# Optimization experiments

Measured on AMD Instinct MI355X. Metric: run time of the kernel, lower is better.

## Reference

```python
import jax, jax.numpy as jnp
import numpy as np

B, L, DIM = 4, 8192, 512
HEADS, WIN = 8, 256
HID = int(DIM * 4.0)
HEAD_DIM = DIM // HEADS
EPS = 1e-5


def _layernorm(x, g, b):
    m = jnp.mean(x, axis=-1, keepdims=True)
    v = jnp.mean(jnp.square(x - m), axis=-1, keepdims=True)
    return (x - m) * jax.lax.rsqrt(v + EPS) * g + b


def setup_inputs() -> dict:
    key = jax.random.key(0)
    ks = jax.random.split(key, 8)
    s = 0.02
    return {
        "x": jax.random.normal(ks[0], (B, L, DIM), jnp.float32),
        "norm1_g": jnp.ones((DIM,), jnp.float32),
        "norm1_b": jnp.zeros((DIM,), jnp.float32),
        "qkv_w": jax.random.normal(ks[1], (DIM, 3 * DIM), jnp.float32) * s,
        "qkv_b": jnp.zeros((3 * DIM,), jnp.float32),
        "rpb_table": jax.random.normal(ks[2], (2 * WIN - 1, HEADS), jnp.float32) * s,
        "proj_w": jax.random.normal(ks[3], (DIM, DIM), jnp.float32) * s,
        "proj_b": jnp.zeros((DIM,), jnp.float32),
        "norm2_g": jnp.ones((DIM,), jnp.float32),
        "norm2_b": jnp.zeros((DIM,), jnp.float32),
        "fc1_w": jax.random.normal(ks[4], (DIM, HID), jnp.float32) * s,
        "fc1_b": jnp.zeros((HID,), jnp.float32),
        "fc2_w": jax.random.normal(ks[5], (HID, DIM), jnp.float32) * s,
        "fc2_b": jnp.zeros((DIM,), jnp.float32),
    }


def reference(x, norm1_g, norm1_b, qkv_w, qkv_b, rpb_table, proj_w, proj_b,
              norm2_g, norm2_b, fc1_w, fc1_b, fc2_w, fc2_b):
    scale = HEAD_DIM ** -0.5
    nW = L // WIN
    BW = B * nW

    shortcut = x
    h = _layernorm(x, norm1_g, norm1_b)
    xw = h.reshape(BW, WIN, DIM)

    qkv = (xw @ qkv_w + qkv_b).reshape(BW, WIN, 3, HEADS, HEAD_DIM)
    q = jnp.moveaxis(qkv[:, :, 0], 1, 2) * scale  # (BW, H, W, d)
    k = jnp.moveaxis(qkv[:, :, 1], 1, 2)
    v = jnp.moveaxis(qkv[:, :, 2], 1, 2)

    attn = jnp.einsum('bhqd,bhkd->bhqk', q, k)
    # relative position bias gather: (W, W, H) -> (H, W, W)
    coords = jnp.arange(WIN)
    ridx = coords[:, None] - coords[None, :] + WIN - 1
    bias = rpb_table[ridx]  # (W, W, H)
    attn = attn + jnp.transpose(bias, (2, 0, 1))[None]
    attn = jax.nn.softmax(attn, axis=-1)

    out = jnp.einsum('bhqk,bhkd->bhqd', attn, v)  # (BW, H, W, d)
    out = jnp.moveaxis(out, 1, 2).reshape(BW, WIN, DIM)
    out = out @ proj_w + proj_b

    x = shortcut + out.reshape(B, L, DIM)
    # NOTE: norm2 output feeds BOTH the residual branch and the MLP (as in source)
    x = _layernorm(x, norm2_g, norm2_b)
    m = jax.nn.gelu(x @ fc1_w + fc1_b, approximate=False) @ fc2_w + fc2_b
    return x + m
```

## Files before the change

### kernel.cpp

```cpp
#include <hip/hip_runtime.h>
#include <hip/hip_bf16.h>
#include <math.h>
#include <stdint.h>


typedef __attribute__((ext_vector_type(8))) __bf16 bf16x8;
typedef __attribute__((ext_vector_type(4))) __bf16 bf16x4;
typedef __attribute__((ext_vector_type(4))) float  f32x4;

#define NTOK  32768
#define DIMC  512
#define HEADS 8
#define WIN   256
#define HD    64
#define HIDC  2048
#define LDP   40

__device__ __forceinline__ void gld16(const __bf16* g, __bf16* l)
{
    __builtin_amdgcn_global_load_lds(
        (const __attribute__((address_space(1))) void*)g,
        (__attribute__((address_space(3))) void*)l, 16, 0, 0);
}

#define DSR(dst, base, off) \
    asm volatile("ds_read_b128 %0, %1 offset:" off : "=v"(dst) : "v"(base))

template<int MODE, int OUTF>
__global__ __launch_bounds__(512, 2) void gemm256(
    const __bf16* __restrict__ A, int lda,
    const __bf16* __restrict__ Bt, int ldb,
    const float* __restrict__ bias,
    const void* __restrict__ res, int res_f32,
    void* __restrict__ C, int ldc, int K,
    int nM, int nN)
{
    __shared__ __bf16 lds[2][2][16384];
    const int tid  = threadIdx.x;
    const int wave = tid >> 6, lane = tid & 63;
    const int quad = lane >> 4, l16 = lane & 15;
    const int wm = wave >> 2, wn = wave & 3;

    const int id  = blockIdx.x;
    const int xcd = id & 7;
    const int lid = id >> 3;
    const int mq  = lid / nN;
    const int mt  = xcd * (nM >> 3) + mq;
    const int nt  = lid - mq * nN;
    const int m0 = mt * 256, n0 = nt * 256;

    int aoff[4], boff[4];
    #pragma unroll
    for (int j = 0; j < 4; j++) {
        const int S = wave * 4 + j;
        const int row = (S >> 1) * 16 + l16;
        const int kof = (S & 1) * 32 + quad * 8;
        aoff[j] = (m0 + row) * lda + kof;
        boff[j] = (n0 + row) * ldb + kof;
    }

    const uint32_t lds0 =
        (uint32_t)(uintptr_t)(__attribute__((address_space(3))) void*)&lds[0][0][0];
    const uint32_t aAd0 = lds0 + wm * 16384 + lane * 16;
    const uint32_t bAd0 = lds0 + 32768 + wn * 8192 + lane * 16;

    f32x4 acc[8][4] = {};
    bf16x8 rA[4][2], rB[4][2];

    const int ntk = K >> 6;

    #pragma unroll
    for (int j = 0; j < 4; j++) {
        gld16(A  + aoff[j], &lds[0][0][(wave * 4 + j) * 512]);
        gld16(Bt + boff[j], &lds[0][1][(wave * 4 + j) * 512]);
    }
    #pragma unroll
    for (int j = 0; j < 4; j++) {
        gld16(A  + aoff[j] + 64, &lds[1][0][(wave * 4 + j) * 512]);
        gld16(Bt + boff[j] + 64, &lds[1][1][(wave * 4 + j) * 512]);
    }
    asm volatile("s_waitcnt vmcnt(8)");
    __builtin_amdgcn_s_barrier();

    for (int t = 0; t < ntk; ++t) {
        const int buf = t & 1;
        const uint32_t aAd = aAd0 + buf * 65536;
        const uint32_t bAd = bAd0 + buf * 65536;
        const bool pf = (t + 2 < ntk);
        const int kn = (t + 2) << 6;

        DSR(rA[0][0], aAd, "0");    DSR(rA[0][1], aAd, "1024");
        DSR(rA[1][0], aAd, "2048"); DSR(rA[1][1], aAd, "3072");
        DSR(rA[2][0], aAd, "4096"); DSR(rA[2][1], aAd, "5120");
        DSR(rA[3][0], aAd, "6144"); DSR(rA[3][1], aAd, "7168");
        DSR(rB[0][0], bAd, "0");    DSR(rB[0][1], bAd, "1024");
        DSR(rB[1][0], bAd, "2048"); DSR(rB[1][1], bAd, "3072");
        __builtin_amdgcn_s_barrier();
        asm volatile("s_waitcnt lgkmcnt(0)");
        __builtin_amdgcn_sched_barrier(0);
        __builtin_amdgcn_s_setprio(1);
        #pragma unroll
        for (int i = 0; i < 4; i++)
            #pragma unroll
            for (int j = 0; j < 2; j++)
                #pragma unroll
                for (int ks = 0; ks < 2; ks++)
                    acc[i][j] = __builtin_amdgcn_mfma_f32_16x16x32_bf16(
                        rB[j][ks], rA[i][ks], acc[i][j], 0, 0, 0);
        __builtin_amdgcn_s_setprio(0);
        __builtin_amdgcn_s_barrier();

        DSR(rB[2][0], bAd, "4096"); DSR(rB[2][1], bAd, "5120");
        DSR(rB[3][0], bAd, "6144"); DSR(rB[3][1], bAd, "7168");
        __builtin_amdgcn_s_barrier();
        asm volatile("s_waitcnt lgkmcnt(0)");
        __builtin_amdgcn_sched_barrier(0);
        __builtin_amdgcn_s_setprio(1);
        #pragma unroll
        for (int i = 0; i < 4; i++)
            #pragma unroll
            for (int j = 2; j < 4; j++)
                #pragma unroll
                for (int ks = 0; ks < 2; ks++)
                    acc[i][j] = __builtin_amdgcn_mfma_f32_16x16x32_bf16(
                        rB[j][ks], rA[i][ks], acc[i][j], 0, 0, 0);
        __builtin_amdgcn_s_setprio(0);
        __builtin_amdgcn_s_barrier();

        DSR(rA[0][0], aAd, "8192");  DSR(rA[0][1], aAd, "9216");
        DSR(rA[1][0], aAd, "10240"); DSR(rA[1][1], aAd, "11264");
        DSR(rA[2][0], aAd, "12288"); DSR(rA[2][1], aAd, "13312");
        DSR(rA[3][0], aAd, "14336"); DSR(rA[3][1], aAd, "15360");
        if (pf) {
            #pragma unroll
            for (int j = 0; j < 4; j++)
                gld16(Bt + boff[j] + kn, &lds[buf][1][(wave * 4 + j) * 512]);
        }
        __builtin_amdgcn_s_barrier();
        asm volatile("s_waitcnt lgkmcnt(0)");
        __builtin_amdgcn_sched_barrier(0);
        __builtin_amdgcn_s_setprio(1);
        #pragma unroll
        for (int i = 0; i < 4; i++)
            #pragma unroll
            for (int j = 0; j < 2; j++)
                #pragma unroll
                for (int ks = 0; ks < 2; ks++)
                    acc[4 + i][j] = __builtin_amdgcn_mfma_f32_16x16x32_bf16(
                        rB[j][ks], rA[i][ks], acc[4 + i][j], 0, 0, 0);
        __builtin_amdgcn_s_setprio(0);
        __builtin_amdgcn_s_barrier();

        if (pf) {
            #pragma unroll
            for (int j = 0; j < 4; j++)
                gld16(A + aoff[j] + kn, &lds[buf][0][(wave * 4 + j) * 512]);
        }
        __builtin_amdgcn_s_setprio(1);
        #pragma unroll
        for (int i = 0; i < 4; i++)
            #pragma unroll
            for (int j = 2; j < 4; j++)
                #pragma unroll
                for (int ks = 0; ks < 2; ks++)
                    acc[4 + i][j] = __builtin_amdgcn_mfma_f32_16x16x32_bf16(
                        rB[j][ks], rA[i][ks], acc[4 + i][j], 0, 0, 0);
        __builtin_amdgcn_s_setprio(0);
        if (pf)                  asm volatile("s_waitcnt vmcnt(8)");
        else if (t + 1 < ntk)    asm volatile("s_waitcnt vmcnt(0)");
        __builtin_amdgcn_s_barrier();
    }

    #pragma unroll
    for (int i = 0; i < 8; i++) {
        const int row = m0 + wm * 128 + i * 16 + l16;
        #pragma unroll
        for (int j = 0; j < 4; j++) {
            const int colb = n0 + wn * 64 + j * 16 + quad * 4;
            const size_t off = (size_t)row * ldc + colb;
            const f32x4 bv = *(const f32x4*)(bias + colb);
            f32x4 v;
            #pragma unroll
            for (int r = 0; r < 4; r++) v[r] = acc[i][j][r] + bv[r];
            if (MODE == 2) {
                #pragma unroll
                for (int r = 0; r < 4; r++)
                    v[r] = 0.5f * v[r] * (1.0f + erff(v[r] * 0.70710678118654752f));
            }
            if (MODE == 1) {
                if (res_f32) {
                    const f32x4 rv = *(const f32x4*)((const float*)res + off);
                    #pragma unroll
                    for (int r = 0; r < 4; r++) v[r] += rv[r];
                } else {
                    const bf16x4 rv = *(const bf16x4*)((const __bf16*)res + off);
                    #pragma unroll
                    for (int r = 0; r < 4; r++) v[r] += (float)rv[r];
                }
            }
            if (OUTF) {
                *(f32x4*)((float*)C + off) = v;
            } else {
                bf16x4 o;
                #pragma unroll
                for (int r = 0; r < 4; r++) o[r] = (__bf16)v[r];
                *(bf16x4*)((__bf16*)C + off) = o;
            }
        }
    }
}

__global__ __launch_bounds__(256) void qk_softmax(
    const __bf16* __restrict__ qkvb, const float* __restrict__ rpb,
    __bf16* __restrict__ Sc, int bh_base)
{
    __shared__ __align__(16) __bf16 Qs[64 * 72];
    __shared__ __align__(16) __bf16 Ks[256 * 72];
    __shared__ float rpbs[320];
    const int bhl = blockIdx.y;
    const int bh  = bh_base + bhl;
    const int bw = bh >> 3, head = bh & 7;
    const int m0 = blockIdx.x * 64;
    const int tid = threadIdx.x;
    const __bf16* qb = qkvb + (size_t)bw * WIN * 1536 + head * HD;

    {
        const int row = tid >> 3, l8 = (tid & 7) * 8;
        #pragma unroll
        for (int p = 0; p < 2; p++) {
            const int r = p * 32 + row;
            *(bf16x8*)(Qs + r * 72 + l8) =
                *(const bf16x8*)(qb + (size_t)(m0 + r) * 1536 + l8);
        }
        #pragma unroll
        for (int p = 0; p < 8; p++) {
            const int r = p * 32 + row;
            *(bf16x8*)(Ks + r * 72 + l8) =
                *(const bf16x8*)(qb + 512 + (size_t)r * 1536 + l8);
        }
        rpbs[tid] = rpb[(size_t)(m0 + tid) * HEADS + head];
        if (tid < 63) rpbs[256 + tid] = rpb[(size_t)(m0 + 256 + tid) * HEADS + head];
    }
    __syncthreads();

    const int wave = tid >> 6, lane = tid & 63;
    const int quad = lane >> 4, l16 = lane & 15;
    bf16x8 af[2];
    #pragma unroll
    for (int ks = 0; ks < 2; ks++)
        af[ks] = *(const bf16x8*)(Qs + (wave * 16 + l16) * 72 + ks * 32 + quad * 8);

    f32x4 acc[16];
    #pragma unroll
    for (int nb = 0; nb < 16; nb++) acc[nb] = (f32x4){0.f, 0.f, 0.f, 0.f};
    #pragma unroll
    for (int nb = 0; nb < 16; nb++) {
        #pragma unroll
        for (int ks = 0; ks < 2; ks++) {
            bf16x8 bf = *(const bf16x8*)(Ks + (nb * 16 + l16) * 72 + ks * 32 + quad * 8);
            acc[nb] = __builtin_amdgcn_mfma_f32_16x16x32_bf16(af[ks], bf, acc[nb], 0, 0, 0);
        }
    }
    #pragma unroll
    for (int nb = 0; nb < 16; nb++)
        #pragma unroll
        for (int r = 0; r < 4; r++) {
            const int li = wave * 16 + quad * 4 + r;
            acc[nb][r] = acc[nb][r] * 0.125f + rpbs[li - nb * 16 - l16 + 255];
        }
    __bf16* Sb = Sc + (size_t)bhl * (WIN * WIN);
    #pragma unroll
    for (int r = 0; r < 4; r++) {
        float m = -1e30f;
        #pragma unroll
        for (int nb = 0; nb < 16; nb++) m = fmaxf(m, acc[nb][r]);
        #pragma unroll
        for (int msk = 1; msk < 16; msk <<= 1) m = fmaxf(m, __shfl_xor(m, msk));
        float s = 0.f;
        #pragma unroll
        for (int nb = 0; nb < 16; nb++) { acc[nb][r] = __expf(acc[nb][r] - m); s += acc[nb][r]; }
        #pragma unroll
        for (int msk = 1; msk < 16; msk <<= 1) s += __shfl_xor(s, msk);
        const float inv = 1.0f / s;
        const int i = m0 + wave * 16 + quad * 4 + r;
        #pragma unroll
        for (int nb = 0; nb < 16; nb++)
            Sb[(size_t)i * WIN + nb * 16 + l16] = (__bf16)(acc[nb][r] * inv);
    }
}

__device__ __forceinline__ void mfma_tile64(
    const __bf16* __restrict__ A, int lda, int m0,
    const __bf16* __restrict__ Bt, int ldb, int n0,
    int K, f32x4* acc, __bf16* As, __bf16* Bs)
{
    const int tid  = threadIdx.x;
    const int wave = tid >> 6;
    const int lane = tid & 63;
    const int quad = lane >> 4;
    const int l16  = lane & 15;
    const int lrow = tid >> 2;
    const int lcol = (tid & 3) << 3;
    const __bf16* ap = A  + (size_t)(m0 + lrow) * lda + lcol;
    const __bf16* bp = Bt + (size_t)(n0 + lrow) * ldb + lcol;
    for (int k0 = 0; k0 < K; k0 += 32) {
        bf16x8 av = *(const bf16x8*)(ap + k0);
        bf16x8 bv = *(const bf16x8*)(bp + k0);
        __syncthreads();
        *(bf16x8*)(As + lrow * LDP + lcol) = av;
        *(bf16x8*)(Bs + lrow * LDP + lcol) = bv;
        __syncthreads();
        bf16x8 af = *(const bf16x8*)(As + (wave * 16 + l16) * LDP + (quad << 3));
        #pragma unroll
        for (int nb = 0; nb < 4; nb++) {
            bf16x8 bf = *(const bf16x8*)(Bs + (nb * 16 + l16) * LDP + (quad << 3));
            acc[nb] = __builtin_amdgcn_mfma_f32_16x16x32_bf16(af, bf, acc[nb], 0, 0, 0);
        }
    }
}

__global__ __launch_bounds__(256) void vtrans(
    const __bf16* __restrict__ qkvb, __bf16* __restrict__ Vt, int bh_base)
{
    __shared__ __align__(16) __bf16 s[WIN * 72];
    const int bh = bh_base + blockIdx.x;
    const int bw = bh >> 3, head = bh & 7;
    const int tid = threadIdx.x;
    const __bf16* V = qkvb + (size_t)bw * WIN * 1536 + 1024 + head * HD;
    #pragma unroll
    for (int it = 0; it < 8; it++) {
        int idx = it * 256 + tid;
        int j = idx >> 3;
        int d0 = (idx & 7) * 8;
        *(bf16x8*)(s + j * 72 + d0) = *(const bf16x8*)(V + (size_t)j * 1536 + d0);
    }
    __syncthreads();
    __bf16* out = Vt + (size_t)blockIdx.x * (HD * WIN);
    #pragma unroll
    for (int it = 0; it < 8; it++) {
        int idx = it * 256 + tid;
        int d  = idx >> 5;
        int j0 = (idx & 31) * 8;
        bf16x8 v;
        #pragma unroll
        for (int j = 0; j < 8; j++) v[j] = s[(j0 + j) * 72 + d];
        *(bf16x8*)(out + (size_t)d * WIN + j0) = v;
    }
}

__global__ __launch_bounds__(256) void pv_gemm(
    const __bf16* __restrict__ Sc, const __bf16* __restrict__ Vt,
    __bf16* __restrict__ attnO, int bh_base)
{
    __shared__ __align__(16) __bf16 As[64 * LDP];
    __shared__ __align__(16) __bf16 Bs[64 * LDP];
    const int bhl = blockIdx.y;
    const int bh = bh_base + bhl;
    const int bw = bh >> 3, head = bh & 7;
    const int m0 = blockIdx.x * 64;
    const __bf16* P   = Sc + (size_t)bhl * (WIN * WIN);
    const __bf16* Vtb = Vt + (size_t)bhl * (HD * WIN);
    f32x4 acc[4] = {};
    mfma_tile64(P, WIN, m0, Vtb, WIN, 0, WIN, acc, As, Bs);
    const int lane = threadIdx.x & 63, wave = threadIdx.x >> 6;
    const int quad = lane >> 4, l16 = lane & 15;
    #pragma unroll
    for (int nb = 0; nb < 4; nb++) {
        const int d = nb * 16 + l16;
        #pragma unroll
        for (int r = 0; r < 4; r++) {
            const int i = m0 + wave * 16 + quad * 4 + r;
            attnO[(size_t)(bw * WIN + i) * DIMC + head * HD + d] = (__bf16)acc[nb][r];
        }
    }
}

__global__ __launch_bounds__(256) void ln_kernel(
    const void* X, int xf,
    const float* __restrict__ g, const float* __restrict__ b,
    __bf16* O)
{
    const int tok  = blockIdx.x * 4 + (threadIdx.x >> 6);
    const int lane = threadIdx.x & 63;
    const size_t base = (size_t)tok * DIMC + lane * 8;
    float v[8];
    if (xf) {
        const float* xp = (const float*)X + base;
        f32x4 a = *(const f32x4*)xp;
        f32x4 c = *(const f32x4*)(xp + 4);
        #pragma unroll
        for (int j = 0; j < 4; j++) { v[j] = a[j]; v[4 + j] = c[j]; }
    } else {
        bf16x8 xv = *(const bf16x8*)((const __bf16*)X + base);
        #pragma unroll
        for (int j = 0; j < 8; j++) v[j] = (float)xv[j];
    }
    float s = 0.f, s2 = 0.f;
    #pragma unroll
    for (int j = 0; j < 8; j++) { s += v[j]; s2 += v[j] * v[j]; }
    #pragma unroll
    for (int off = 32; off; off >>= 1) { s += __shfl_xor(s, off); s2 += __shfl_xor(s2, off); }
    const float mean = s * (1.0f / DIMC);
    const float var  = s2 * (1.0f / DIMC) - mean * mean;
    const float rstd = rsqrtf(var + 1e-5f);
    f32x4 ga = *(const f32x4*)(g + lane * 8);
    f32x4 gc = *(const f32x4*)(g + lane * 8 + 4);
    f32x4 ba = *(const f32x4*)(b + lane * 8);
    f32x4 bc = *(const f32x4*)(b + lane * 8 + 4);
    bf16x8 ov;
    #pragma unroll
    for (int j = 0; j < 4; j++) {
        ov[j]     = (__bf16)((v[j]     - mean) * rstd * ga[j] + ba[j]);
        ov[4 + j] = (__bf16)((v[4 + j] - mean) * rstd * gc[j] + bc[j]);
    }
    *(bf16x8*)(O + base) = ov;
}

__global__ __launch_bounds__(256) void wtrans(
    const float* __restrict__ W, __bf16* __restrict__ Wt, int K, int N)
{
    __shared__ __align__(16) __bf16 s[64 * 72];
    const int kb = blockIdx.y * 64, nb = blockIdx.x * 64;
    const int tid = threadIdx.x;
    #pragma unroll
    for (int it = 0; it < 2; it++) {
        int idx = it * 256 + tid;
        int lk = idx >> 3;
        int ln = (idx & 7) * 8;
        const float* wp = W + (size_t)(kb + lk) * N + nb + ln;
        f32x4 a = *(const f32x4*)wp;
        f32x4 c = *(const f32x4*)(wp + 4);
        bf16x8 v;
        #pragma unroll
        for (int j = 0; j < 4; j++) { v[j] = (__bf16)a[j]; v[4 + j] = (__bf16)c[j]; }
        *(bf16x8*)(s + lk * 72 + ln) = v;
    }
    __syncthreads();
    #pragma unroll
    for (int it = 0; it < 2; it++) {
        int idx = it * 256 + tid;
        int ln  = idx >> 3;
        int lkv = (idx & 7) * 8;
        bf16x8 v;
        #pragma unroll
        for (int j = 0; j < 8; j++) v[j] = s[(lkv + j) * 72 + ln];
        *(bf16x8*)(Wt + (size_t)(nb + ln) * K + kb + lkv) = v;
    }
}

extern "C" void kernel_launch(void* const* d_in, const int* in_sizes, int n_in,
                              void* d_out, int out_size, void* d_ws, size_t ws_size,
                              hipStream_t stream)
{
    const float* x      = (const float*)d_in[0];
    const float* n1g    = (const float*)d_in[1];
    const float* n1b    = (const float*)d_in[2];
    const float* qkv_w  = (const float*)d_in[3];
    const float* qkv_b  = (const float*)d_in[4];
    const float* rpb    = (const float*)d_in[5];
    const float* proj_w = (const float*)d_in[6];
    const float* proj_b = (const float*)d_in[7];
    const float* n2g    = (const float*)d_in[8];
    const float* n2b    = (const float*)d_in[9];
    const float* fc1_w  = (const float*)d_in[10];
    const float* fc1_b  = (const float*)d_in[11];
    const float* fc2_w  = (const float*)d_in[12];
    const float* fc2_b  = (const float*)d_in[13];
    float* out = (float*)d_out;

    char* ws = (char*)d_ws;
    __bf16* qkvb  = (__bf16*)(ws + 0);
    __bf16* hid   = (__bf16*)(ws + 0);
    __bf16* h     = (__bf16*)(ws + 134217728);
    __bf16* Sc    = h;
    __bf16* y     = h;
    __bf16* attnO = (__bf16*)(ws + 167772160);
    __bf16* Vt    = (__bf16*)(ws + 201326592);
    __bf16* wq_t  = (__bf16*)(ws + 209715200);
    __bf16* wp_t  = (__bf16*)(ws + 211288064);
    __bf16* w1_t  = (__bf16*)(ws + 211812352);
    __bf16* w2_t  = (__bf16*)(ws + 213909504);

    wtrans<<<dim3(1536 / 64, 512 / 64),  256, 0, stream>>>(qkv_w, wq_t, 512, 1536);
    wtrans<<<dim3(512 / 64,  512 / 64),  256, 0, stream>>>(proj_w, wp_t, 512, 512);
    wtrans<<<dim3(2048 / 64, 512 / 64),  256, 0, stream>>>(fc1_w, w1_t, 512, 2048);
    wtrans<<<dim3(512 / 64,  2048 / 64), 256, 0, stream>>>(fc2_w, w2_t, 2048, 512);

    ln_kernel<<<NTOK / 4, 256, 0, stream>>>(x, 1, n1g, n1b, h);

    gemm256<0, 0><<<768, 512, 0, stream>>>(
        h, DIMC, wq_t, DIMC, qkv_b, nullptr, 0, qkvb, 1536, DIMC, 128, 6);

    for (int c = 0; c < 4; c++) {
        const int bh0 = c * 256;
        vtrans<<<256, 256, 0, stream>>>(qkvb, Vt, bh0);
        qk_softmax<<<dim3(4, 256), 256, 0, stream>>>(qkvb, rpb, Sc, bh0);
        pv_gemm<<<dim3(4, 256), 256, 0, stream>>>(Sc, Vt, attnO, bh0);
    }

    gemm256<1, 0><<<256, 512, 0, stream>>>(
        attnO, DIMC, wp_t, DIMC, proj_b, x, 1, y, DIMC, DIMC, 128, 2);

    ln_kernel<<<NTOK / 4, 256, 0, stream>>>(y, 0, n2g, n2b, y);

    gemm256<2, 0><<<1024, 512, 0, stream>>>(
        y, DIMC, w1_t, DIMC, fc1_b, nullptr, 0, hid, HIDC, DIMC, 128, 8);

    gemm256<1, 1><<<256, 512, 0, stream>>>(
        hid, HIDC, w2_t, HIDC, fc2_b, y, 0, out, DIMC, HIDC, 128, 2);
}
```

Measured before the change: 680.1 us.

## Fuse QK-softmax with PV matmul, keeping probabilities in swizzled LDS

```diff
diff --git a/kernel.cpp b/kernel.cpp
--- a/kernel.cpp
+++ b/kernel.cpp
@@ -14,7 +14,6 @@
 #define WIN   256
 #define HD    64
 #define HIDC  2048
-#define LDP   40
 
 __device__ __forceinline__ void gld16(const __bf16* g, __bf16* l)
 {
@@ -210,15 +209,14 @@
     }
 }
 
-__global__ __launch_bounds__(256) void qk_softmax(
+__global__ __launch_bounds__(256) void attn_fused(
     const __bf16* __restrict__ qkvb, const float* __restrict__ rpb,
-    __bf16* __restrict__ Sc, int bh_base)
+    const __bf16* __restrict__ Vt, __bf16* __restrict__ attnO)
 {
     __shared__ __align__(16) __bf16 Qs[64 * 72];
     __shared__ __align__(16) __bf16 Ks[256 * 72];
     __shared__ float rpbs[320];
-    const int bhl = blockIdx.y;
-    const int bh  = bh_base + bhl;
+    const int bh = blockIdx.y;
     const int bw = bh >> 3, head = bh & 7;
     const int m0 = blockIdx.x * 64;
     const int tid = threadIdx.x;
@@ -268,7 +266,10 @@
             const int li = wave * 16 + quad * 4 + r;
             acc[nb][r] = acc[nb][r] * 0.125f + rpbs[li - nb * 16 - l16 + 255];
         }
-    __bf16* Sb = Sc + (size_t)bhl * (WIN * WIN);
+
+    __syncthreads();
+
+    char* Pb = (char*)Ks;
     #pragma unroll
     for (int r = 0; r < 4; r++) {
         float m = -1e30f;
@@ -282,39 +283,41 @@
         #pragma unroll
         for (int msk = 1; msk < 16; msk <<= 1) s += __shfl_xor(s, msk);
         const float inv = 1.0f / s;
-        const int i = m0 + wave * 16 + quad * 4 + r;
-        #pragma unroll
-        for (int nb = 0; nb < 16; nb++)
-            Sb[(size_t)i * WIN + nb * 16 + l16] = (__bf16)(acc[nb][r] * inv);
-    }
-}
-
-__device__ __forceinline__ void mfma_tile64(
-    const __bf16* __restrict__ A, int lda, int m0,
-    const __bf16* __restrict__ Bt, int ldb, int n0,
-    int K, f32x4* acc, __bf16* As, __bf16* Bs)
-{
-    const int tid  = threadIdx.x;
-    const int wave = tid >> 6;
-    const int lane = tid & 63;
-    const int quad = lane >> 4;
-    const int l16  = lane & 15;
-    const int lrow = tid >> 2;
-    const int lcol = (tid & 3) << 3;
-    const __bf16* ap = A  + (size_t)(m0 + lrow) * lda + lcol;
-    const __bf16* bp = Bt + (size_t)(n0 + lrow) * ldb + lcol;
-    for (int k0 = 0; k0 < K; k0 += 32) {
-        bf16x8 av = *(const bf16x8*)(ap + k0);
-        bf16x8 bv = *(const bf16x8*)(bp + k0);
-        __syncthreads();
-        *(bf16x8*)(As + lrow * LDP + lcol) = av;
-        *(bf16x8*)(Bs + lrow * LDP + lcol) = bv;
-        __syncthreads();
-        bf16x8 af = *(const bf16x8*)(As + (wave * 16 + l16) * LDP + (quad << 3));
-        #pragma unroll
-        for (int nb = 0; nb < 4; nb++) {
-            bf16x8 bf = *(const bf16x8*)(Bs + (nb * 16 + l16) * LDP + (quad << 3));
-            acc[nb] = __builtin_amdgcn_mfma_f32_16x16x32_bf16(af, bf, acc[nb], 0, 0, 0);
+        const int row = wave * 16 + quad * 4 + r;
+        const int rx = row & 7;
+        #pragma unroll
+        for (int nb = 0; nb < 16; nb++) {
+            const int c = nb * 2 + (l16 >> 3);
+            *(__bf16*)(Pb + row * 512 + ((c ^ rx) << 4) + ((l16 & 7) << 1)) =
+                (__bf16)(acc[nb][r] * inv);
+        }
+    }
+    __syncthreads();
+
+    const __bf16* Vtb = Vt + (size_t)bh * (HD * WIN);
+    const int prow = wave * 16 + l16;
+    const int px = prow & 7;
+    f32x4 acc2[4] = {};
+    #pragma unroll
+    for (int ks2 = 0; ks2 < 8; ks2++) {
+        const bf16x8 pa = *(const bf16x8*)(Pb + prow * 512
+                                + (((ks2 * 4 + quad) ^ px) << 4));
+        #pragma unroll
+        for (int nb2 = 0; nb2 < 4; nb2++) {
+            const bf16x8 vf = *(const bf16x8*)(Vtb + (size_t)(nb2 * 16 + l16) * WIN
+                                + ks2 * 32 + quad * 8);
+            acc2[nb2] = __builtin_amdgcn_mfma_f32_16x16x32_bf16(vf, pa, acc2[nb2], 0, 0, 0);
+        }
+    }
+    {
+        const int i = m0 + wave * 16 + l16;
+        __bf16* ob = attnO + (size_t)(bw * WIN + i) * DIMC + head * HD;
+        #pragma unroll
+        for (int nb2 = 0; nb2 < 4; nb2++) {
+            bf16x4 o;
+            #pragma unroll
+            for (int r = 0; r < 4; r++) o[r] = (__bf16)acc2[nb2][r];
+            *(bf16x4*)(ob + nb2 * 16 + quad * 4) = o;
         }
     }
 }
@@ -345,33 +348,6 @@
         #pragma unroll
         for (int j = 0; j < 8; j++) v[j] = s[(j0 + j) * 72 + d];
         *(bf16x8*)(out + (size_t)d * WIN + j0) = v;
-    }
-}
-
-__global__ __launch_bounds__(256) void pv_gemm(
-    const __bf16* __restrict__ Sc, const __bf16* __restrict__ Vt,
-    __bf16* __restrict__ attnO, int bh_base)
-{
-    __shared__ __align__(16) __bf16 As[64 * LDP];
-    __shared__ __align__(16) __bf16 Bs[64 * LDP];
-    const int bhl = blockIdx.y;
-    const int bh = bh_base + bhl;
-    const int bw = bh >> 3, head = bh & 7;
-    const int m0 = blockIdx.x * 64;
-    const __bf16* P   = Sc + (size_t)bhl * (WIN * WIN);
-    const __bf16* Vtb = Vt + (size_t)bhl * (HD * WIN);
-    f32x4 acc[4] = {};
-    mfma_tile64(P, WIN, m0, Vtb, WIN, 0, WIN, acc, As, Bs);
-    const int lane = threadIdx.x & 63, wave = threadIdx.x >> 6;
-    const int quad = lane >> 4, l16 = lane & 15;
-    #pragma unroll
-    for (int nb = 0; nb < 4; nb++) {
-        const int d = nb * 16 + l16;
-        #pragma unroll
-        for (int r = 0; r < 4; r++) {
-            const int i = m0 + wave * 16 + quad * 4 + r;
-            attnO[(size_t)(bw * WIN + i) * DIMC + head * HD + d] = (__bf16)acc[nb][r];
-        }
     }
 }
 
@@ -471,11 +447,10 @@
     char* ws = (char*)d_ws;
     __bf16* qkvb  = (__bf16*)(ws + 0);
     __bf16* hid   = (__bf16*)(ws + 0);
+    __bf16* Vt    = (__bf16*)(ws + 100663296);
     __bf16* h     = (__bf16*)(ws + 134217728);
-    __bf16* Sc    = h;
     __bf16* y     = h;
     __bf16* attnO = (__bf16*)(ws + 167772160);
-    __bf16* Vt    = (__bf16*)(ws + 201326592);
     __bf16* wq_t  = (__bf16*)(ws + 209715200);
     __bf16* wp_t  = (__bf16*)(ws + 211288064);
     __bf16* w1_t  = (__bf16*)(ws + 211812352);
@@ -491,12 +466,8 @@
     gemm256<0, 0><<<768, 512, 0, stream>>>(
         h, DIMC, wq_t, DIMC, qkv_b, nullptr, 0, qkvb, 1536, DIMC, 128, 6);
 
-    for (int c = 0; c < 4; c++) {
-        const int bh0 = c * 256;
-        vtrans<<<256, 256, 0, stream>>>(qkvb, Vt, bh0);
-        qk_softmax<<<dim3(4, 256), 256, 0, stream>>>(qkvb, rpb, Sc, bh0);
-        pv_gemm<<<dim3(4, 256), 256, 0, stream>>>(Sc, Vt, attnO, bh0);
-    }
+    vtrans<<<1024, 256, 0, stream>>>(qkvb, Vt, 0);
+    attn_fused<<<dim3(4, 1024), 256, 0, stream>>>(qkvb, rpb, Vt, attnO);
 
     gemm256<1, 0><<<256, 512, 0, stream>>>(
         attnO, DIMC, wp_t, DIMC, proj_b, x, 1, y, DIMC, DIMC, 128, 2);
```

Result: faster. 640.7 us, median of 2 (-5.8%).
